# Kernel tuning notes

Measured on AMD Instinct MI355X. Metric: run time of the kernel, lower is better.

The kernel has to match this reference:

```python
import jax, jax.numpy as jnp
import numpy as np

NCHAR, NHID, NSTACK, STACK, DEPTH, T = 256, 2048, 32, 512, 4, 4096
TOP = 0  # top_of_stack


def _xavier(k, shape):
    fan_in, fan_out = shape[-1], shape[-2]
    std = (2.0 / (fan_in + fan_out)) ** 0.5
    return (jax.random.normal(k, shape) * std).astype(jnp.float32)


def setup_inputs() -> dict:
    key = jax.random.key(0)
    ks = jax.random.split(key, 7)
    in2hid_w = _xavier(ks[0], (NHID, NCHAR))
    hid2hid_w = _xavier(ks[1], (NHID, NHID))  # mod=2 -> xavier, not zeros
    hid2act_w = _xavier(ks[2], (NSTACK, 3, NHID))
    # init zero-masks: hid2stack rows below TOP+1 kept, rest zero; stack2hid cols >= DEPTH zero
    hid2stack_w = _xavier(ks[3], (NSTACK, STACK, NHID)).at[:, TOP + 1:, :].set(0.0)
    stack2hid_w = _xavier(ks[4], (NSTACK, NHID, STACK)).at[:, :, TOP + DEPTH:].set(0.0)
    hid2out_w = _xavier(ks[5], (NCHAR, NHID))
    tokens = jax.random.randint(ks[6], (T,), 0, NCHAR, dtype=jnp.int32)
    return dict(tokens=tokens, in2hid_w=in2hid_w, hid2hid_w=hid2hid_w,
                hid2act_w=hid2act_w, hid2stack_w=hid2stack_w,
                stack2hid_w=stack2hid_w, hid2out_w=hid2out_w)


def reference(tokens, in2hid_w, hid2hid_w, hid2act_w, hid2stack_w, stack2hid_w, hid2out_w):
    """Sequential StackRNN (mod=2, use_noop=True, soft actions) over T tokens.
    Shift-matrix matmuls replaced by equivalent O(n) rolls (push/pop/noop
    matrices with TOP=0 are exactly shift-down / shift-up / identity).
    Returns per-step output probabilities [T, NCHAR]."""
    neg_one_col = jnp.full((NSTACK, 1), -1.0, jnp.float32)

    def step(carry, x_t):
        hidden, stacks = carry  # [NHID], [NSTACK, STACK]
        # h = U x_t + sum_s P_s s_{t-1}[:depth] + R h_{t-1}
        h = in2hid_w[:, x_t]
        h = h + jnp.einsum('snd,sd->n', stack2hid_w[:, :, TOP:TOP + DEPTH],
                           stacks[:, TOP:TOP + DEPTH])
        h = h + hid2hid_w @ hidden
        h = jax.nn.sigmoid(h)
        # per-stack action distribution: [pop, push, noop]
        acts = jax.nn.softmax(jnp.einsum('san,n->sa', hid2act_w, h), axis=-1)
        pop_w, push_w, noop_w = acts[:, 0:1], acts[:, 1:2], acts[:, 2:3]
        # pushed top value (only row TOP of hid2stack is used)
        top_val = jax.nn.sigmoid(jnp.clip(hid2stack_w[:, TOP, :] @ h, -50.0, 50.0))  # [NSTACK]
        pushed = jnp.concatenate([top_val[:, None], stacks[:, :-1]], axis=1)
        popped = jnp.concatenate([stacks[:, 1:], neg_one_col], axis=1)
        new_stacks = push_w * pushed + pop_w * popped + noop_w * stacks
        probs = jax.nn.softmax(hid2out_w @ h)
        return (h, new_stacks), probs

    hidden0 = jnp.zeros((NHID,), jnp.float32)
    stacks0 = jnp.full((NSTACK, STACK), -1.0, jnp.float32)
    _, out = jax.lax.scan(step, (hidden0, stacks0), tokens)
    return out  # [T, NCHAR]
```

## Files before the change

kernel.cpp:

```cpp
#include <hip/hip_runtime.h>
#include <math.h>

#define NCHAR 256
#define NHID 2048
#define NSTACK 32
#define STACK 512
#define T 4096
#define NB 128
#define BT 512
#define RPB 16
#define AGENT __HIP_MEMORY_SCOPE_AGENT

__device__ __forceinline__ float cohLoadF(const float* p) {
  return __hip_atomic_load(p, __ATOMIC_RELAXED, AGENT);
}
__device__ __forceinline__ void cohStoreF(float* p, float v) {
  __hip_atomic_store(p, v, __ATOMIC_RELAXED, AGENT);
}
__device__ __forceinline__ float4 cohLoad4(const float4* p) {
  float4 r;
  asm volatile("global_load_dwordx4 %0, %1, off sc0 sc1\n\ts_waitcnt vmcnt(0)"
               : "=&v"(r) : "v"(p) : "memory");
  return r;
}

__global__ __launch_bounds__(BT) void stackrnn_seq(
    const int* __restrict__ tokens,
    const float* __restrict__ in2hid,
    const float* __restrict__ hid2hid,
    const float* __restrict__ hid2act,
    const float* __restrict__ hid2stack,
    const float* __restrict__ stack2hid,
    const float* __restrict__ hid2out,
    float* __restrict__ out,
    float* __restrict__ Hbuf,
    float* __restrict__ Lred,
    float* __restrict__ TopsG,
    float* __restrict__ Halo,
    int*   __restrict__ flag1,
    int*   __restrict__ flag2)
{
  __shared__ int    sTok[T];
  __shared__ float4 sH[576];
  __shared__ float  sActs[NSTACK][3];
  __shared__ float  sTopv[NSTACK];
  __shared__ float  sTops[NSTACK][4];
  __shared__ float  sSt[2][128];
  __shared__ float  sRed[8][3];

  const int tid = threadIdx.x;
  const int b   = blockIdx.x;
  const int wv  = tid >> 6;
  const int l   = tid & 63;
  const int r0  = b * RPB + 2 * wv;
  const int r1  = r0 + 1;

  float wA[32], wB[32];
  {
    const float4* pa = (const float4*)(hid2hid + (size_t)r0 * NHID + 32 * l);
    const float4* pb = (const float4*)(hid2hid + (size_t)r1 * NHID + 32 * l);
#pragma unroll
    for (int j = 0; j < 8; ++j) {
      float4 v = pa[j];
      wA[4*j] = v.x; wA[4*j+1] = v.y; wA[4*j+2] = v.z; wA[4*j+3] = v.w;
    }
#pragma unroll
    for (int j = 0; j < 8; ++j) {
      float4 v = pb[j];
      wB[4*j] = v.x; wB[4*j+1] = v.y; wB[4*j+2] = v.z; wB[4*j+3] = v.w;
    }
  }
  const float* lrow = (b < 96) ? (hid2act + (size_t)b * NHID)
                               : (hid2stack + (size_t)(b - 96) * STACK * NHID);
  const float4 wl  = ((const float4*)lrow)[tid];
  const float4 wo0 = ((const float4*)(hid2out + (size_t)(2 * b) * NHID))[tid];
  const float4 wo1 = ((const float4*)(hid2out + (size_t)(2 * b + 1) * NHID))[tid];
  const int cs = l >> 1, cd = (l & 1) * 2;
  float w2a0, w2a1, w2b0, w2b1;
  {
    const float* p = stack2hid + (size_t)cs * NHID * STACK;
    w2a0 = p[(size_t)r0 * STACK + cd]; w2a1 = p[(size_t)r0 * STACK + cd + 1];
    w2b0 = p[(size_t)r1 * STACK + cd]; w2b1 = p[(size_t)r1 * STACK + cd + 1];
  }

  for (int i = tid; i < T; i += BT) sTok[i] = tokens[i];

  const int bs = b >> 2;
  const int bd = (b & 3) * 128 + (tid - 384);
  float bval = -1.f;

  __syncthreads();

#pragma unroll 1
  for (int w = 0; w < T; ++w) {
    const int pw_ = w & 1, pr_ = pw_ ^ 1;
    const int xt  = sTok[w];
    const float e0 = in2hid[(size_t)r0 * NCHAR + xt];
    const float e1 = in2hid[(size_t)r1 * NCHAR + xt];

    if (w > 0 && wv == 0) {
      int v0, v1;
      do {
        v0 = __hip_atomic_load(&flag2[l],      __ATOMIC_RELAXED, AGENT);
        v1 = __hip_atomic_load(&flag2[64 + l], __ATOMIC_RELAXED, AGENT);
      } while (__any(v0 < w || v1 < w));
    }
    __syncthreads();

    float la0 = 0.f, la1 = 0.f, la2 = 0.f, lt = 0.f;
    float tg0 = 0.f, tg1 = 0.f, tg2 = 0.f, tg3 = 0.f, tg4 = 0.f;
    if (w > 0 && tid < NSTACK) {
      la0 = cohLoadF(&Lred[3 * tid]);
      la1 = cohLoadF(&Lred[3 * tid + 1]);
      la2 = cohLoadF(&Lred[3 * tid + 2]);
      lt  = cohLoadF(&Lred[96 + tid]);
      const float* tg = TopsG + ((size_t)pr_ * NSTACK + tid) * 5;
      tg0 = cohLoadF(tg);     tg1 = cohLoadF(tg + 1); tg2 = cohLoadF(tg + 2);
      tg3 = cohLoadF(tg + 3); tg4 = cohLoadF(tg + 4);
    }
    float hlv = 0.f, hrv = -1.f;
    if (w > 0) {
      if (tid == 384 && (b & 3) != 0) hlv = cohLoadF(&Halo[((size_t)pr_ * NB + b - 1) * 2 + 1]);
      if (tid == 511 && (b & 3) != 3) hrv = cohLoadF(&Halo[((size_t)pr_ * NB + b + 1) * 2]);
    }

    float acc0 = 0.f, acc1 = 0.f;
    if (w > 0) {
#pragma unroll
      for (int j = 0; j < 8; ++j) {
        const float4 hv = sH[9 * l + j];
        acc0 += wA[4*j]*hv.x + wA[4*j+1]*hv.y + wA[4*j+2]*hv.z + wA[4*j+3]*hv.w;
        acc1 += wB[4*j]*hv.x + wB[4*j+1]*hv.y + wB[4*j+2]*hv.z + wB[4*j+3]*hv.w;
      }
    }

    if (tid < NSTACK) {
      if (w > 0) {
        const float m  = fmaxf(la0, fmaxf(la1, la2));
        const float ea = expf(la0 - m), eb = expf(la1 - m), ec = expf(la2 - m);
        const float inv = 1.f / (ea + eb + ec);
        const float qw = ea * inv, pwt = eb * inv, nw = ec * inv;
        sActs[tid][0] = qw; sActs[tid][1] = pwt; sActs[tid][2] = nw;
        float tv = fminf(50.f, fmaxf(-50.f, lt));
        tv = 1.f / (1.f + expf(-tv));
        sTopv[tid] = tv;
        sTops[tid][0] = pwt * tv  + qw * tg1 + nw * tg0;
        sTops[tid][1] = pwt * tg0 + qw * tg2 + nw * tg1;
        sTops[tid][2] = pwt * tg1 + qw * tg3 + nw * tg2;
        sTops[tid][3] = pwt * tg2 + qw * tg4 + nw * tg3;
      } else {
        sActs[tid][0] = sActs[tid][1] = sActs[tid][2] = 0.f;
        sTopv[tid] = 0.f;
        sTops[tid][0] = sTops[tid][1] = sTops[tid][2] = sTops[tid][3] = -1.f;
      }
    }
    __syncthreads();

    acc0 += w2a0 * sTops[cs][cd] + w2a1 * sTops[cs][cd + 1];
    acc1 += w2b0 * sTops[cs][cd] + w2b1 * sTops[cs][cd + 1];
#pragma unroll
    for (int m = 1; m < 64; m <<= 1) {
      acc0 += __shfl_xor(acc0, m);
      acc1 += __shfl_xor(acc1, m);
    }
    const float h0 = 1.f / (1.f + expf(-(acc0 + e0)));
    const float h1 = 1.f / (1.f + expf(-(acc1 + e1)));
    if (l == 0) {
      cohStoreF(&Hbuf[(size_t)pw_ * NHID + r0], h0);
      cohStoreF(&Hbuf[(size_t)pw_ * NHID + r1], h1);
    }

    if (tid >= 384) {
      float nv;
      if (w > 0) {
        const int j = tid - 384;
        const float leftRaw = (tid == 384) ? hlv : sSt[pr_][j - 1];
        const float pushed  = (bd == 0) ? sTopv[bs] : leftRaw;
        const float popped  = (tid == 511) ? hrv : sSt[pr_][j + 1];
        nv = sActs[bs][1] * pushed + sActs[bs][0] * popped + sActs[bs][2] * bval;
      } else {
        nv = -1.f;
      }
      bval = nv;
      sSt[pw_][tid - 384] = nv;
      if (tid == 384) cohStoreF(&Halo[((size_t)pw_ * NB + b) * 2 + 0], nv);
      if (tid == 511) cohStoreF(&Halo[((size_t)pw_ * NB + b) * 2 + 1], nv);
      if ((b & 3) == 0 && tid <= 388)
        cohStoreF(&TopsG[((size_t)pw_ * NSTACK + bs) * 5 + (tid - 384)], nv);
    }
    __syncthreads();
    if (tid == 0)
      __hip_atomic_store(&flag1[b], w + 1, __ATOMIC_RELAXED, AGENT);

    if (wv == 0) {
      int v0, v1;
      do {
        v0 = __hip_atomic_load(&flag1[l],      __ATOMIC_RELAXED, AGENT);
        v1 = __hip_atomic_load(&flag1[64 + l], __ATOMIC_RELAXED, AGENT);
      } while (__any(v0 <= w || v1 <= w));
    }
    __syncthreads();

    const float4 hv4 = cohLoad4((const float4*)(Hbuf + (size_t)pw_ * NHID) + tid);
    sH[tid + (tid >> 3)] = hv4;
    float d0 = wl.x  * hv4.x + wl.y  * hv4.y + wl.z  * hv4.z + wl.w  * hv4.w;
    float d1 = wo0.x * hv4.x + wo0.y * hv4.y + wo0.z * hv4.z + wo0.w * hv4.w;
    float d2 = wo1.x * hv4.x + wo1.y * hv4.y + wo1.z * hv4.z + wo1.w * hv4.w;
#pragma unroll
    for (int m = 1; m < 64; m <<= 1) {
      d0 += __shfl_xor(d0, m);
      d1 += __shfl_xor(d1, m);
      d2 += __shfl_xor(d2, m);
    }
    if (l == 0) { sRed[wv][0] = d0; sRed[wv][1] = d1; sRed[wv][2] = d2; }
    __syncthreads();
    if (tid == 0) {
      float s0 = 0.f, s1 = 0.f, s2 = 0.f;
#pragma unroll
      for (int g = 0; g < 8; ++g) {
        s0 += sRed[g][0]; s1 += sRed[g][1]; s2 += sRed[g][2];
      }
      cohStoreF(&Lred[b], s0);
      cohStoreF(&out[(size_t)w * NCHAR + 2 * b],     s1);
      cohStoreF(&out[(size_t)w * NCHAR + 2 * b + 1], s2);
      asm volatile("s_waitcnt vmcnt(0)" ::: "memory");
      __hip_atomic_store(&flag2[b], w + 1, __ATOMIC_RELAXED, AGENT);
    }
  }
}

__global__ __launch_bounds__(64) void row_softmax(float* __restrict__ out) {
  const int t = blockIdx.x;
  const int l = threadIdx.x;
  float4* p = (float4*)(out + (size_t)t * NCHAR);
  float4 v = p[l];
  float m = fmaxf(fmaxf(v.x, v.y), fmaxf(v.z, v.w));
#pragma unroll
  for (int k = 1; k < 64; k <<= 1) m = fmaxf(m, __shfl_xor(m, k));
  const float ex = expf(v.x - m), ey = expf(v.y - m);
  const float ez = expf(v.z - m), ew = expf(v.w - m);
  float s = ex + ey + ez + ew;
#pragma unroll
  for (int k = 1; k < 64; k <<= 1) s += __shfl_xor(s, k);
  const float inv = 1.f / s;
  p[l] = make_float4(ex * inv, ey * inv, ez * inv, ew * inv);
}

extern "C" void kernel_launch(void* const* d_in, const int* in_sizes, int n_in,
                              void* d_out, int out_size, void* d_ws, size_t ws_size,
                              hipStream_t stream) {
  const int*   tokens    = (const int*)d_in[0];
  const float* in2hid    = (const float*)d_in[1];
  const float* hid2hid   = (const float*)d_in[2];
  const float* hid2act   = (const float*)d_in[3];
  const float* hid2stack = (const float*)d_in[4];
  const float* stack2hid = (const float*)d_in[5];
  const float* hid2out   = (const float*)d_in[6];
  float* out = (float*)d_out;

  float* ws    = (float*)d_ws;
  float* Hbuf  = ws;
  float* Lred  = Hbuf + 2 * NHID;
  float* TopsG = Lred + 128;
  float* Halo  = TopsG + 320;
  int*   flag1 = (int*)(Halo + 512);
  int*   flag2 = flag1 + NB;

  hipLaunchKernelGGL(stackrnn_seq, dim3(NB), dim3(BT), 0, stream,
                     tokens, in2hid, hid2hid, hid2act, hid2stack, stack2hid,
                     hid2out, out, Hbuf, Lred, TopsG, Halo, flag1, flag2);
  hipLaunchKernelGGL(row_softmax, dim3(T), dim3(64), 0, stream, out);
}
```

Measured before the change: 41.41 ms.

## Use one grid barrier per step with partial-logit exchange and fewer, larger blocks

The persistent recurrent kernel drops from two grid-wide flag barriers per timestep to one. Each block now computes partial action/top logits from its own hidden rows and publishes them to a partial buffer, which every block sums after the barrier. The output projection is deferred by one step and uses the shared hidden copy, with a final epilogue for the last step. Blocks go from 128×512 threads to 64×1024, so each whole stack lives in one block and the halo exchange disappears. In exchange, every block must read all partials each step (64×128 loads) and each block adds more __syncthreads calls.

```diff
diff --git a/kernel.cpp b/kernel.cpp
--- a/kernel.cpp
+++ b/kernel.cpp
@@ -6,9 +6,9 @@
 #define NSTACK 32
 #define STACK 512
 #define T 4096
-#define NB 128
-#define BT 512
-#define RPB 16
+#define NB 64
+#define BT 1024
+#define RPB 32
 #define AGENT __HIP_MEMORY_SCOPE_AGENT
 
 __device__ __forceinline__ float cohLoadF(const float* p) {
@@ -16,12 +16,6 @@
 }
 __device__ __forceinline__ void cohStoreF(float* p, float v) {
   __hip_atomic_store(p, v, __ATOMIC_RELAXED, AGENT);
-}
-__device__ __forceinline__ float4 cohLoad4(const float4* p) {
-  float4 r;
-  asm volatile("global_load_dwordx4 %0, %1, off sc0 sc1\n\ts_waitcnt vmcnt(0)"
-               : "=&v"(r) : "v"(p) : "memory");
-  return r;
 }
 
 __global__ __launch_bounds__(BT) void stackrnn_seq(
@@ -34,19 +28,21 @@
     const float* __restrict__ hid2out,
     float* __restrict__ out,
     float* __restrict__ Hbuf,
-    float* __restrict__ Lred,
+    float* __restrict__ Pbuf,
     float* __restrict__ TopsG,
-    float* __restrict__ Halo,
-    int*   __restrict__ flag1,
-    int*   __restrict__ flag2)
+    int*   __restrict__ flags)
 {
   __shared__ int    sTok[T];
   __shared__ float4 sH[576];
+  __shared__ float  sLpart[4][128];
+  __shared__ float  sL[128];
+  __shared__ float  sTgL[160];
   __shared__ float  sActs[NSTACK][3];
   __shared__ float  sTopv[NSTACK];
   __shared__ float  sTops[NSTACK][4];
-  __shared__ float  sSt[2][128];
-  __shared__ float  sRed[8][3];
+  __shared__ float  sSt[2][STACK];
+  __shared__ float  sLl[16][128];
+  __shared__ float  sOut[16];
 
   const int tid = threadIdx.x;
   const int b   = blockIdx.x;
@@ -70,11 +66,16 @@
       wB[4*j] = v.x; wB[4*j+1] = v.y; wB[4*j+2] = v.z; wB[4*j+3] = v.w;
     }
   }
-  const float* lrow = (b < 96) ? (hid2act + (size_t)b * NHID)
-                               : (hid2stack + (size_t)(b - 96) * STACK * NHID);
-  const float4 wl  = ((const float4*)lrow)[tid];
-  const float4 wo0 = ((const float4*)(hid2out + (size_t)(2 * b) * NHID))[tid];
-  const float4 wo1 = ((const float4*)(hid2out + (size_t)(2 * b + 1) * NHID))[tid];
+  float wl00, wl01, wl10, wl11;
+  {
+    const int lg0 = 2 * l, lg1 = 2 * l + 1;
+    const float* p0 = (lg0 < 96) ? (hid2act + (size_t)lg0 * NHID)
+                                 : (hid2stack + (size_t)(lg0 - 96) * STACK * NHID);
+    const float* p1 = (lg1 < 96) ? (hid2act + (size_t)lg1 * NHID)
+                                 : (hid2stack + (size_t)(lg1 - 96) * STACK * NHID);
+    wl00 = p0[r0]; wl01 = p0[r1];
+    wl10 = p1[r0]; wl11 = p1[r1];
+  }
   const int cs = l >> 1, cd = (l & 1) * 2;
   float w2a0, w2a1, w2b0, w2b1;
   {
@@ -82,11 +83,19 @@
     w2a0 = p[(size_t)r0 * STACK + cd]; w2a1 = p[(size_t)r0 * STACK + cd + 1];
     w2b0 = p[(size_t)r1 * STACK + cd]; w2b1 = p[(size_t)r1 * STACK + cd + 1];
   }
+  const int ocol = 4 * b + (wv & 3);
+  const int oseg = wv >> 2;
+  float wo[8];
+  {
+    const float4* p = (const float4*)(hid2out + (size_t)ocol * NHID + oseg * 512 + 8 * l);
+    float4 v0 = p[0], v1 = p[1];
+    wo[0] = v0.x; wo[1] = v0.y; wo[2] = v0.z; wo[3] = v0.w;
+    wo[4] = v1.x; wo[5] = v1.y; wo[6] = v1.z; wo[7] = v1.w;
+  }
 
   for (int i = tid; i < T; i += BT) sTok[i] = tokens[i];
 
-  const int bs = b >> 2;
-  const int bd = (b & 3) * 128 + (tid - 384);
+  const int sOwn = b >> 1;
   float bval = -1.f;
 
   __syncthreads();
@@ -95,35 +104,38 @@
   for (int w = 0; w < T; ++w) {
     const int pw_ = w & 1, pr_ = pw_ ^ 1;
     const int xt  = sTok[w];
+
+    if (w > 0 && wv == 0) {
+      int v;
+      do {
+        v = __hip_atomic_load(&flags[l], __ATOMIC_RELAXED, AGENT);
+      } while (__any(v < w));
+    }
+    __syncthreads();
+
+    if (w > 0) {
+      if (tid >= 512) {
+        const int u = tid - 512;
+        const float* hb = Hbuf + (size_t)pr_ * NHID + 4 * u;
+        float a0 = cohLoadF(hb), a1 = cohLoadF(hb + 1);
+        float a2 = cohLoadF(hb + 2), a3 = cohLoadF(hb + 3);
+        sH[u + (u >> 3)] = make_float4(a0, a1, a2, a3);
+      } else {
+        const int k = tid >> 7, j = tid & 127;
+        const float* pp = Pbuf + (size_t)pr_ * NB * 128 + (size_t)(16 * k) * 128 + j;
+        float s = 0.f;
+#pragma unroll
+        for (int q = 0; q < 16; ++q) s += cohLoadF(pp + q * 128);
+        sLpart[k][j] = s;
+        if (tid < 160) sTgL[tid] = cohLoadF(&TopsG[(size_t)pr_ * 160 + tid]);
+      }
+    }
     const float e0 = in2hid[(size_t)r0 * NCHAR + xt];
     const float e1 = in2hid[(size_t)r1 * NCHAR + xt];
-
-    if (w > 0 && wv == 0) {
-      int v0, v1;
-      do {
-        v0 = __hip_atomic_load(&flag2[l],      __ATOMIC_RELAXED, AGENT);
-        v1 = __hip_atomic_load(&flag2[64 + l], __ATOMIC_RELAXED, AGENT);
-      } while (__any(v0 < w || v1 < w));
-    }
-    __syncthreads();
-
-    float la0 = 0.f, la1 = 0.f, la2 = 0.f, lt = 0.f;
-    float tg0 = 0.f, tg1 = 0.f, tg2 = 0.f, tg3 = 0.f, tg4 = 0.f;
-    if (w > 0 && tid < NSTACK) {
-      la0 = cohLoadF(&Lred[3 * tid]);
-      la1 = cohLoadF(&Lred[3 * tid + 1]);
-      la2 = cohLoadF(&Lred[3 * tid + 2]);
-      lt  = cohLoadF(&Lred[96 + tid]);
-      const float* tg = TopsG + ((size_t)pr_ * NSTACK + tid) * 5;
-      tg0 = cohLoadF(tg);     tg1 = cohLoadF(tg + 1); tg2 = cohLoadF(tg + 2);
-      tg3 = cohLoadF(tg + 3); tg4 = cohLoadF(tg + 4);
-    }
-    float hlv = 0.f, hrv = -1.f;
-    if (w > 0) {
-      if (tid == 384 && (b & 3) != 0) hlv = cohLoadF(&Halo[((size_t)pr_ * NB + b - 1) * 2 + 1]);
-      if (tid == 511 && (b & 3) != 3) hrv = cohLoadF(&Halo[((size_t)pr_ * NB + b + 1) * 2]);
-    }
-
+    __syncthreads();
+
+    if (w > 0 && tid < 128)
+      sL[tid] = sLpart[0][tid] + sLpart[1][tid] + sLpart[2][tid] + sLpart[3][tid];
     float acc0 = 0.f, acc1 = 0.f;
     if (w > 0) {
 #pragma unroll
@@ -133,17 +145,22 @@
         acc1 += wB[4*j]*hv.x + wB[4*j+1]*hv.y + wB[4*j+2]*hv.z + wB[4*j+3]*hv.w;
       }
     }
+    __syncthreads();
 
     if (tid < NSTACK) {
       if (w > 0) {
+        const float la0 = sL[3 * tid], la1 = sL[3 * tid + 1], la2 = sL[3 * tid + 2];
         const float m  = fmaxf(la0, fmaxf(la1, la2));
         const float ea = expf(la0 - m), eb = expf(la1 - m), ec = expf(la2 - m);
         const float inv = 1.f / (ea + eb + ec);
         const float qw = ea * inv, pwt = eb * inv, nw = ec * inv;
         sActs[tid][0] = qw; sActs[tid][1] = pwt; sActs[tid][2] = nw;
-        float tv = fminf(50.f, fmaxf(-50.f, lt));
+        float tv = fminf(50.f, fmaxf(-50.f, sL[96 + tid]));
         tv = 1.f / (1.f + expf(-tv));
         sTopv[tid] = tv;
+        const float tg0 = sTgL[tid * 5],     tg1 = sTgL[tid * 5 + 1];
+        const float tg2 = sTgL[tid * 5 + 2], tg3 = sTgL[tid * 5 + 3];
+        const float tg4 = sTgL[tid * 5 + 4];
         sTops[tid][0] = pwt * tv  + qw * tg1 + nw * tg0;
         sTops[tid][1] = pwt * tg0 + qw * tg2 + nw * tg1;
         sTops[tid][2] = pwt * tg1 + qw * tg3 + nw * tg2;
@@ -169,64 +186,73 @@
       cohStoreF(&Hbuf[(size_t)pw_ * NHID + r0], h0);
       cohStoreF(&Hbuf[(size_t)pw_ * NHID + r1], h1);
     }
-
-    if (tid >= 384) {
+    sLl[wv][2 * l]     = wl00 * h0 + wl01 * h1;
+    sLl[wv][2 * l + 1] = wl10 * h0 + wl11 * h1;
+
+    if ((b & 1) == 0 && tid >= 512) {
+      const int d = tid - 512;
       float nv;
       if (w > 0) {
-        const int j = tid - 384;
-        const float leftRaw = (tid == 384) ? hlv : sSt[pr_][j - 1];
-        const float pushed  = (bd == 0) ? sTopv[bs] : leftRaw;
-        const float popped  = (tid == 511) ? hrv : sSt[pr_][j + 1];
-        nv = sActs[bs][1] * pushed + sActs[bs][0] * popped + sActs[bs][2] * bval;
+        const float left   = (d > 0) ? sSt[pr_][d - 1] : 0.f;
+        const float pushed = (d == 0) ? sTopv[sOwn] : left;
+        const float popped = (d < STACK - 1) ? sSt[pr_][d + 1] : -1.f;
+        nv = sActs[sOwn][1] * pushed + sActs[sOwn][0] * popped + sActs[sOwn][2] * bval;
       } else {
         nv = -1.f;
       }
       bval = nv;
-      sSt[pw_][tid - 384] = nv;
-      if (tid == 384) cohStoreF(&Halo[((size_t)pw_ * NB + b) * 2 + 0], nv);
-      if (tid == 511) cohStoreF(&Halo[((size_t)pw_ * NB + b) * 2 + 1], nv);
-      if ((b & 3) == 0 && tid <= 388)
-        cohStoreF(&TopsG[((size_t)pw_ * NSTACK + bs) * 5 + (tid - 384)], nv);
-    }
+      sSt[pw_][d] = nv;
+      if (d < 5) cohStoreF(&TopsG[(size_t)pw_ * 160 + sOwn * 5 + d], nv);
+    }
+
+    if (w > 0) {
+      const int f0 = oseg * 128 + 2 * l;
+      const float4 hv0 = sH[f0 + (f0 >> 3)];
+      const float4 hv1 = sH[(f0 + 1) + ((f0 + 1) >> 3)];
+      float dv = wo[0]*hv0.x + wo[1]*hv0.y + wo[2]*hv0.z + wo[3]*hv0.w
+               + wo[4]*hv1.x + wo[5]*hv1.y + wo[6]*hv1.z + wo[7]*hv1.w;
+#pragma unroll
+      for (int m = 1; m < 64; m <<= 1) dv += __shfl_xor(dv, m);
+      if (l == 0) sOut[wv] = dv;
+    }
+    __syncthreads();
+
+    if (tid < 128) {
+      float pv = 0.f;
+#pragma unroll
+      for (int g = 0; g < 16; ++g) pv += sLl[g][tid];
+      cohStoreF(&Pbuf[(size_t)pw_ * NB * 128 + (size_t)b * 128 + tid], pv);
+    }
+    if (w > 0 && tid < 4)
+      out[(size_t)(w - 1) * NCHAR + 4 * b + tid] =
+          sOut[tid] + sOut[4 + tid] + sOut[8 + tid] + sOut[12 + tid];
+
+    asm volatile("s_waitcnt vmcnt(0)" ::: "memory");
     __syncthreads();
     if (tid == 0)
-      __hip_atomic_store(&flag1[b], w + 1, __ATOMIC_RELAXED, AGENT);
-
-    if (wv == 0) {
-      int v0, v1;
-      do {
-        v0 = __hip_atomic_load(&flag1[l],      __ATOMIC_RELAXED, AGENT);
-        v1 = __hip_atomic_load(&flag1[64 + l], __ATOMIC_RELAXED, AGENT);
-      } while (__any(v0 <= w || v1 <= w));
-    }
-    __syncthreads();
-
-    const float4 hv4 = cohLoad4((const float4*)(Hbuf + (size_t)pw_ * NHID) + tid);
-    sH[tid + (tid >> 3)] = hv4;
-    float d0 = wl.x  * hv4.x + wl.y  * hv4.y + wl.z  * hv4.z + wl.w  * hv4.w;
-    float d1 = wo0.x * hv4.x + wo0.y * hv4.y + wo0.z * hv4.z + wo0.w * hv4.w;
-    float d2 = wo1.x * hv4.x + wo1.y * hv4.y + wo1.z * hv4.z + wo1.w * hv4.w;
-#pragma unroll
-    for (int m = 1; m < 64; m <<= 1) {
-      d0 += __shfl_xor(d0, m);
-      d1 += __shfl_xor(d1, m);
-      d2 += __shfl_xor(d2, m);
-    }
-    if (l == 0) { sRed[wv][0] = d0; sRed[wv][1] = d1; sRed[wv][2] = d2; }
-    __syncthreads();
-    if (tid == 0) {
-      float s0 = 0.f, s1 = 0.f, s2 = 0.f;
-#pragma unroll
-      for (int g = 0; g < 8; ++g) {
-        s0 += sRed[g][0]; s1 += sRed[g][1]; s2 += sRed[g][2];
-      }
-      cohStoreF(&Lred[b], s0);
-      cohStoreF(&out[(size_t)w * NCHAR + 2 * b],     s1);
-      cohStoreF(&out[(size_t)w * NCHAR + 2 * b + 1], s2);
-      asm volatile("s_waitcnt vmcnt(0)" ::: "memory");
-      __hip_atomic_store(&flag2[b], w + 1, __ATOMIC_RELAXED, AGENT);
-    }
-  }
+      __hip_atomic_store(&flags[b], w + 1, __ATOMIC_RELAXED, AGENT);
+  }
+
+  if (wv == 0) {
+    int v;
+    do {
+      v = __hip_atomic_load(&flags[l], __ATOMIC_RELAXED, AGENT);
+    } while (__any(v < T));
+  }
+  __syncthreads();
+  {
+    const float* hb = Hbuf + (size_t)((T - 1) & 1) * NHID + oseg * 512 + 8 * l;
+    float dv = 0.f;
+#pragma unroll
+    for (int e = 0; e < 8; ++e) dv += wo[e] * cohLoadF(hb + e);
+#pragma unroll
+    for (int m = 1; m < 64; m <<= 1) dv += __shfl_xor(dv, m);
+    if (l == 0) sOut[wv] = dv;
+  }
+  __syncthreads();
+  if (tid < 4)
+    out[(size_t)(T - 1) * NCHAR + 4 * b + tid] =
+        sOut[tid] + sOut[4 + tid] + sOut[8 + tid] + sOut[12 + tid];
 }
 
 __global__ __launch_bounds__(64) void row_softmax(float* __restrict__ out) {
@@ -260,14 +286,12 @@
 
   float* ws    = (float*)d_ws;
   float* Hbuf  = ws;
-  float* Lred  = Hbuf + 2 * NHID;
-  float* TopsG = Lred + 128;
-  float* Halo  = TopsG + 320;
-  int*   flag1 = (int*)(Halo + 512);
-  int*   flag2 = flag1 + NB;
+  float* Pbuf  = Hbuf + 2 * NHID;
+  float* TopsG = Pbuf + 2 * NB * 128;
+  int*   flags = (int*)(TopsG + 320);
 
   hipLaunchKernelGGL(stackrnn_seq, dim3(NB), dim3(BT), 0, stream,
                      tokens, in2hid, hid2hid, hid2act, hid2stack, stack2hid,
-                     hid2out, out, Hbuf, Lred, TopsG, Halo, flag1, flag2);
+                     hid2out, out, Hbuf, Pbuf, TopsG, flags);
   hipLaunchKernelGGL(row_softmax, dim3(T), dim3(64), 0, stream, out);
 }
```

Measured after the change: 56.61 ms. 36.7% more time.
